# Kernel optimization log

Measured on AMD Instinct MI355X. Metric: run time of the kernel, lower is better.

Reference implementation:

```python
import jax, jax.numpy as jnp
import numpy as np

N_NODES = 100000


def gcn_conv(x, W, b, src, dst, norm, n_nodes):
    # x: [N, F_in] -> [N, F_out]; GCNConv: D^-1/2 (A+I) D^-1/2 (X W) + b
    h = x @ W                                   # [N, F_out]
    msg = h[src] * norm[:, None]                # [E+N, F_out] gather + scale
    out = jax.ops.segment_sum(msg, dst, num_segments=n_nodes)  # scatter-add
    return out + b


def setup_inputs() -> dict:
    key = jax.random.key(0)
    k0, k1, k2, k3, k4, k5 = jax.random.split(key, 6)
    n, e, f_in, f_hid, n_cls = N_NODES, 1600000, 128, 128, 3
    x = jax.random.normal(k0, (n, f_in), dtype=jnp.float32)
    edge_index = jax.random.randint(k1, (2, e), 0, n, dtype=jnp.int64)
    s1 = 1.0 / np.sqrt(f_in)
    s2 = 1.0 / np.sqrt(f_hid)
    W1 = jax.random.uniform(k2, (f_in, f_hid), jnp.float32, -s1, s1)
    b1 = jnp.zeros((f_hid,), jnp.float32)
    W2 = jax.random.uniform(k3, (f_hid, f_hid), jnp.float32, -s2, s2)
    b2 = jnp.zeros((f_hid,), jnp.float32)
    Wfc = jax.random.uniform(k4, (f_hid, n_cls), jnp.float32, -s2, s2)
    bfc = jax.random.uniform(k5, (n_cls,), jnp.float32, -s2, s2)
    return {"x": x, "edge_index": edge_index, "W1": W1, "b1": b1,
            "W2": W2, "b2": b2, "Wfc": Wfc, "bfc": bfc}


def reference(x, edge_index, W1, b1, W2, b2, Wfc, bfc):
    n = x.shape[0]
    # add self-loops (PyG GCNConv default add_self_loops=True)
    loops = jnp.arange(n, dtype=edge_index.dtype)
    src = jnp.concatenate([edge_index[0], loops])
    dst = jnp.concatenate([edge_index[1], loops])
    deg = jax.ops.segment_sum(jnp.ones_like(dst, dtype=x.dtype), dst,
                              num_segments=n)
    dinv = jax.lax.rsqrt(deg)                   # deg >= 1 due to self-loops
    norm = dinv[src] * dinv[dst]                # [E+N]
    h = jax.nn.relu(gcn_conv(x, W1, b1, src, dst, norm, n))   # dropout=eval id
    h = jax.nn.relu(gcn_conv(h, W2, b2, src, dst, norm, n))
    return jnp.tanh(h @ Wfc + bfc)              # [N, 3]
```

## Files before the change

### kernel.cpp

```cpp
#include <hip/hip_runtime.h>
#include <hip/hip_bf16.h>
#include <hip/hip_fp16.h>


#define NODE_F 128

typedef __attribute__((ext_vector_type(8))) short bf16x8;
typedef __attribute__((ext_vector_type(8))) unsigned short u16x8;
typedef __attribute__((ext_vector_type(4))) float f32x4;

__device__ inline unsigned short bf16_rn(float x) {
    unsigned u = __builtin_bit_cast(unsigned, x);
    unsigned r = (u + 0x7fffu + ((u >> 16) & 1u)) >> 16;
    return (unsigned short)r;
}
__device__ inline float bf16_to_f(unsigned short h) {
    unsigned u = (unsigned)h << 16;
    return __builtin_bit_cast(float, u);
}
__device__ inline void acc8_h(float a[8], uint4 v, float s) {
    unsigned vv[4] = {v.x, v.y, v.z, v.w};
    #pragma unroll
    for (int j = 0; j < 4; ++j) {
        float2 f = __half22float2(__builtin_bit_cast(__half2, vv[j]));
        a[2 * j]     += f.x * s;
        a[2 * j + 1] += f.y * s;
    }
}


__global__ __launch_bounds__(256) void wconv_kernel(const float* __restrict__ W1,
                                                    const float* __restrict__ W2,
                                                    unsigned short* __restrict__ WhiT,
                                                    unsigned short* __restrict__ WloT)
{
    const float* W = blockIdx.x ? W2 : W1;
    unsigned short* hiT = WhiT + blockIdx.x * 128 * 128;
    unsigned short* loT = WloT + blockIdx.x * 128 * 128;
    int tid = threadIdx.x;
    for (int i = tid; i < 128 * 128; i += 256) {
        int k = i >> 7, n = i & 127;
        float x = W[i];
        unsigned short hi = bf16_rn(x);
        float lo = x - bf16_to_f(hi);
        hiT[n * 128 + k] = hi;
        loT[n * 128 + k] = bf16_rn(lo);
    }
}


__global__ __launch_bounds__(256) void scan_block_kernel(
    const int* __restrict__ degE, int* __restrict__ rsA,
    int* __restrict__ bsum, int N)
{
    __shared__ int s[256];
    const int tid = threadIdx.x;
    const int idx = blockIdx.x * 1024 + tid * 4;
    int v0 = (idx + 0 < N) ? degE[idx + 0] : 0;
    int v1 = (idx + 1 < N) ? degE[idx + 1] : 0;
    int v2 = (idx + 2 < N) ? degE[idx + 2] : 0;
    int v3 = (idx + 3 < N) ? degE[idx + 3] : 0;
    int t = v0 + v1 + v2 + v3;
    s[tid] = t;
    __syncthreads();
    #pragma unroll
    for (int off = 1; off < 256; off <<= 1) {
        int x = (tid >= off) ? s[tid - off] : 0;
        __syncthreads();
        s[tid] += x;
        __syncthreads();
    }
    int excl = s[tid] - t;
    if (idx + 0 < N) rsA[idx + 0] = excl;
    if (idx + 1 < N) rsA[idx + 1] = excl + v0;
    if (idx + 2 < N) rsA[idx + 2] = excl + v0 + v1;
    if (idx + 3 < N) rsA[idx + 3] = excl + v0 + v1 + v2;
    if (tid == 255) bsum[blockIdx.x] = s[255];
}

__global__ __launch_bounds__(1024) void scan_tops_kernel(int* __restrict__ bsum, int nb) {
    __shared__ int s[1024];
    const int tid = threadIdx.x;
    int v = (tid < nb) ? bsum[tid] : 0;
    s[tid] = v;
    __syncthreads();
    #pragma unroll
    for (int off = 1; off < 1024; off <<= 1) {
        int x = (tid >= off) ? s[tid - off] : 0;
        __syncthreads();
        s[tid] += x;
        __syncthreads();
    }
    if (tid < nb) bsum[tid] = s[tid] - v;
}


__global__ __launch_bounds__(256) void finish_fill_kernel(
    const int* __restrict__ src, const int* __restrict__ dst,
    const unsigned short* __restrict__ rank,
    const int* __restrict__ rsA, const int* __restrict__ bsum,
    int* __restrict__ rsB, float* __restrict__ dinv,
    const int* __restrict__ degE, int* __restrict__ csr_src,
    int E, int N, int fill_blocks)
{
    if ((int)blockIdx.x < fill_blocks) {
        int e = blockIdx.x * 256 + threadIdx.x;
        if (e < E) {
            int d = dst[e];
            csr_src[rsA[d] + bsum[d >> 10] + (int)rank[e]] = src[e];
        }
    } else {
        int i = (blockIdx.x - fill_blocks) * 256 + threadIdx.x;
        if (i < N) {
            int rs = rsA[i] + bsum[i >> 10];
            rsB[i] = rs;
            dinv[i] = rsqrtf((float)degE[i] + 1.0f);
            if (i == N - 1) rsB[N] = rs + degE[i];
        }
    }
}


template<bool SCALE_OUT>
__device__ __forceinline__ void gemm_compute(
    const unsigned short* __restrict__ WhiT, const unsigned short* __restrict__ WloT,
    const float* __restrict__ dinv, __half* __restrict__ Hout, int N, int rbase,
    unsigned short* xhi, unsigned short* xlo)
{
    const int tid  = threadIdx.x;
    const int lane = tid & 63;
    const int w    = tid >> 6;

    bf16x8 bhi[2][4], blo[2][4];
    {
        int n0   = w * 32 + (lane & 15);
        int koct = (lane >> 4) * 8;
        #pragma unroll
        for (int nt = 0; nt < 2; ++nt) {
            #pragma unroll
            for (int kk = 0; kk < 4; ++kk) {
                size_t o = (size_t)(n0 + nt * 16) * 128 + kk * 32 + koct;
                bhi[nt][kk] = *reinterpret_cast<const bf16x8*>(WhiT + o);
                blo[nt][kk] = *reinterpret_cast<const bf16x8*>(WloT + o);
            }
        }
    }

    f32x4 acc[4][2];
    #pragma unroll
    for (int m = 0; m < 4; ++m)
        #pragma unroll
        for (int nt = 0; nt < 2; ++nt)
            acc[m][nt] = (f32x4){0.f, 0.f, 0.f, 0.f};

    #pragma unroll
    for (int kk = 0; kk < 4; ++kk) {
        #pragma unroll
        for (int m = 0; m < 4; ++m) {
            int row  = m * 16 + (lane & 15);
            int koff = kk * 64 + (lane >> 4) * 16;
            int byte = row * 256 + (koff ^ ((row & 7) << 4));
            bf16x8 ahi = *reinterpret_cast<const bf16x8*>(reinterpret_cast<char*>(xhi) + byte);
            bf16x8 alo = *reinterpret_cast<const bf16x8*>(reinterpret_cast<char*>(xlo) + byte);
            #pragma unroll
            for (int nt = 0; nt < 2; ++nt) {
                acc[m][nt] = __builtin_amdgcn_mfma_f32_16x16x32_bf16(ahi, bhi[nt][kk], acc[m][nt], 0, 0, 0);
                acc[m][nt] = __builtin_amdgcn_mfma_f32_16x16x32_bf16(ahi, blo[nt][kk], acc[m][nt], 0, 0, 0);
                acc[m][nt] = __builtin_amdgcn_mfma_f32_16x16x32_bf16(alo, bhi[nt][kk], acc[m][nt], 0, 0, 0);
            }
        }
    }

    #pragma unroll
    for (int m = 0; m < 4; ++m) {
        int row = rbase + m * 16 + (lane >> 4) * 4;
        int col = w * 32 + (lane & 15);
        #pragma unroll
        for (int nt = 0; nt < 2; ++nt) {
            #pragma unroll
            for (int r = 0; r < 4; ++r) {
                if (row + r < N) {
                    float v = acc[m][nt][r];
                    if (SCALE_OUT) v *= dinv[row + r];
                    Hout[(size_t)(row + r) * NODE_F + col + nt * 16] = __float2half(v);
                }
            }
        }
    }
}


__device__ __forceinline__ void gemm1_body(
    const float* __restrict__ Xf,
    const unsigned short* __restrict__ WhiT, const unsigned short* __restrict__ WloT,
    __half* __restrict__ Hout, int N, int bid,
    unsigned short* xhi, unsigned short* xlo)
{
    const int tid   = threadIdx.x;
    const int rbase = bid * 64;

    #pragma unroll
    for (int it = 0; it < 8; ++it) {
        int f   = it * 256 + tid;
        int row = f >> 5;
        int k4  = f & 31;
        float4 v = make_float4(0.f, 0.f, 0.f, 0.f);
        if (rbase + row < N)
            v = *reinterpret_cast<const float4*>(Xf + (size_t)(rbase + row) * NODE_F + k4 * 4);
        float xs[4] = {v.x, v.y, v.z, v.w};
        ushort4 h4, l4;
        unsigned short* hp = &h4.x;
        unsigned short* lp = &l4.x;
        #pragma unroll
        for (int j = 0; j < 4; ++j) {
            unsigned short hi = bf16_rn(xs[j]);
            hp[j] = hi;
            lp[j] = bf16_rn(xs[j] - bf16_to_f(hi));
        }
        int byte = row * 256 + ((k4 * 8) ^ ((row & 7) << 4));
        *reinterpret_cast<ushort4*>(reinterpret_cast<char*>(xhi) + byte) = h4;
        *reinterpret_cast<ushort4*>(reinterpret_cast<char*>(xlo) + byte) = l4;
    }
    __syncthreads();
    gemm_compute<false>(WhiT, WloT, nullptr, Hout, N, rbase, xhi, xlo);
}


__global__ __launch_bounds__(256) void gemm1deg_kernel(
    const int* __restrict__ dst, int* __restrict__ degE,
    unsigned short* __restrict__ rank, int E,
    int edge_blocks, int gemm_blocks,
    const float* __restrict__ X, const unsigned short* __restrict__ WhiT,
    const unsigned short* __restrict__ WloT, __half* __restrict__ H, int N)
{
    __shared__ unsigned short xhi[64 * 128];
    __shared__ unsigned short xlo[64 * 128];
    int q = blockIdx.x / 5, r = blockIdx.x % 5;
    if (r == 4) {
        int stride = edge_blocks * 256;
        for (int e = q * 256 + threadIdx.x; e < E; e += stride)
            rank[e] = (unsigned short)atomicAdd(&degE[dst[e]], 1);
    } else {
        int gid = q * 4 + r;
        if (gid < gemm_blocks)
            gemm1_body(X, WhiT, WloT, H, N, gid, xhi, xlo);
    }
}


template<bool EDGE_SCALE>
__device__ __forceinline__ void gather_core(
    const __half* __restrict__ Hs, const int* __restrict__ csr_src,
    const int* __restrict__ row_start, const float* __restrict__ dinv,
    int node, int ql, int qi, float a[8])
{
    const char* Hb = reinterpret_cast<const char*>(Hs);
    #pragma unroll
    for (int j = 0; j < 8; ++j) a[j] = 0.f;
    if (qi == 0) {
        float ds = EDGE_SCALE ? dinv[node] : 1.0f;
        acc8_h(a, *reinterpret_cast<const uint4*>(Hb + ((size_t)node * 256 + ql * 16)), ds);
    }

    int i   = row_start[node];
    int end = row_start[node + 1];
    for (; i + 7 < end; i += 8) {
        int s0 = csr_src[i + qi];
        int s1 = csr_src[i + 4 + qi];
        float d0 = EDGE_SCALE ? dinv[s0] : 1.0f;
        float d1 = EDGE_SCALE ? dinv[s1] : 1.0f;
        uint4 v0 = *reinterpret_cast<const uint4*>(Hb + ((size_t)s0 * 256 + ql * 16));
        uint4 v1 = *reinterpret_cast<const uint4*>(Hb + ((size_t)s1 * 256 + ql * 16));
        acc8_h(a, v0, d0);
        acc8_h(a, v1, d1);
    }
    for (; i < end; i += 4) {
        if (i + qi < end) {
            int s = csr_src[i + qi];
            float ds = EDGE_SCALE ? dinv[s] : 1.0f;
            acc8_h(a, *reinterpret_cast<const uint4*>(Hb + ((size_t)s * 256 + ql * 16)), ds);
        }
    }
    #pragma unroll
    for (int j = 0; j < 8; ++j) {
        a[j] += __shfl_xor(a[j], 32);
        a[j] += __shfl_xor(a[j], 16);
    }
}


__global__ __launch_bounds__(256) void gather1_kernel(
    const __half* __restrict__ H, const int* __restrict__ csr_src,
    const int* __restrict__ row_start, const float* __restrict__ dinv,
    const float* __restrict__ b, __half* __restrict__ A1, int N)
{
    int node = (blockIdx.x * blockDim.x + threadIdx.x) >> 6;
    int lane = threadIdx.x & 63;
    int ql = lane & 15, qi = lane >> 4;
    if (node >= N) return;

    float a[8];
    gather_core<true>(H, csr_src, row_start, dinv, node, ql, qi, a);

    if (qi == 0) {
        const float dd = dinv[node];
        u16x8 o;
        #pragma unroll
        for (int j = 0; j < 8; ++j) {
            float r = fmaxf(b[ql * 8 + j] + dd * a[j], 0.f);
            o[j] = __builtin_bit_cast(unsigned short, __float2half(r));
        }
        *reinterpret_cast<u16x8*>(reinterpret_cast<char*>(A1) + ((size_t)node * 256 + ql * 16)) = o;
    }
}


__global__ __launch_bounds__(256) void gemm2_kernel(
    const __half* __restrict__ A1,
    const unsigned short* __restrict__ WhiT, const unsigned short* __restrict__ WloT,
    const float* __restrict__ dinv, __half* __restrict__ Hs, int N)
{
    __shared__ unsigned short xhi[64 * 128];
    __shared__ unsigned short xlo[64 * 128];
    const int tid   = threadIdx.x;
    const int rbase = blockIdx.x * 64;

    #pragma unroll
    for (int it = 0; it < 4; ++it) {
        int idx = it * 256 + tid;
        int row = idx >> 4;
        int k8  = idx & 15;
        u16x8 h = {0, 0, 0, 0, 0, 0, 0, 0};
        u16x8 l = {0, 0, 0, 0, 0, 0, 0, 0};
        if (rbase + row < N) {
            u16x8 v = *reinterpret_cast<const u16x8*>(
                reinterpret_cast<const char*>(A1) + ((size_t)(rbase + row) * 256 + k8 * 16));
            #pragma unroll
            for (int j = 0; j < 8; ++j) {
                float f = __half2float(__builtin_bit_cast(__half, (unsigned short)v[j]));
                unsigned short hi = bf16_rn(f);
                h[j] = hi;
                l[j] = bf16_rn(f - bf16_to_f(hi));
            }
        }
        int byte = row * 256 + ((k8 * 16) ^ ((row & 7) << 4));
        *reinterpret_cast<u16x8*>(reinterpret_cast<char*>(xhi) + byte) = h;
        *reinterpret_cast<u16x8*>(reinterpret_cast<char*>(xlo) + byte) = l;
    }
    __syncthreads();
    gemm_compute<true>(WhiT, WloT, dinv, Hs, N, rbase, xhi, xlo);
}


__global__ __launch_bounds__(256) void gather2fc_kernel(
    const __half* __restrict__ Hs, const int* __restrict__ csr_src,
    const int* __restrict__ row_start, const float* __restrict__ dinv,
    const float* __restrict__ b, const float* __restrict__ Wfc,
    const float* __restrict__ bfc, float* __restrict__ out, int N)
{
    int node = (blockIdx.x * blockDim.x + threadIdx.x) >> 6;
    int lane = threadIdx.x & 63;
    int ql = lane & 15, qi = lane >> 4;
    if (node >= N) return;

    float a[8];
    gather_core<false>(Hs, csr_src, row_start, dinv, node, ql, qi, a);

    const float dd = dinv[node];
    float p0 = 0.f, p1 = 0.f, p2 = 0.f;
    #pragma unroll
    for (int j = 0; j < 8; ++j) {
        float r = fmaxf(b[ql * 8 + j] + dd * a[j], 0.f);
        const float* wr = Wfc + (size_t)(ql * 8 + j) * 3;
        p0 += r * wr[0]; p1 += r * wr[1]; p2 += r * wr[2];
    }
    #pragma unroll
    for (int off = 8; off > 0; off >>= 1) {
        p0 += __shfl_down(p0, off);
        p1 += __shfl_down(p1, off);
        p2 += __shfl_down(p2, off);
    }
    if (lane == 0) {
        out[(size_t)node * 3 + 0] = tanhf(p0 + bfc[0]);
        out[(size_t)node * 3 + 1] = tanhf(p1 + bfc[1]);
        out[(size_t)node * 3 + 2] = tanhf(p2 + bfc[2]);
    }
}

extern "C" void kernel_launch(void* const* d_in, const int* in_sizes, int n_in,
                              void* d_out, int out_size, void* d_ws, size_t ws_size,
                              hipStream_t stream)
{
    const float* x    = (const float*)d_in[0];
    const int*   edge = (const int*)d_in[1];
    const float* W1   = (const float*)d_in[2];
    const float* b1   = (const float*)d_in[3];
    const float* W2   = (const float*)d_in[4];
    const float* b2   = (const float*)d_in[5];
    const float* Wfc  = (const float*)d_in[6];
    const float* bfc  = (const float*)d_in[7];
    float* out = (float*)d_out;

    const int N = in_sizes[0] / NODE_F;
    const int E = in_sizes[1] / 2;
    const int* src = edge;
    const int* dst = edge + E;

    char* ws = (char*)d_ws;
    size_t off = 0;
    auto alloc = [&](size_t bytes) {
        void* p = ws + off;
        off += (bytes + 511) & ~511ull;
        return p;
    };
    const int nblk = (N + 1023) / 1024;
    float* dinv      = (float*)alloc((size_t)N * 4);
    int*   degE      = (int*)  alloc((size_t)N * 4);
    unsigned short* rank = (unsigned short*)alloc((size_t)E * 2);
    int*   rsA       = (int*)  alloc((size_t)N * 4);
    int*   rsB       = (int*)  alloc((size_t)(N + 1) * 4);
    int*   bsum      = (int*)  alloc((size_t)nblk * 4);
    int*   csr_src   = (int*)  alloc((size_t)E * 4);
    unsigned short* WhiT = (unsigned short*)alloc(2 * 128 * 128 * 2);
    unsigned short* WloT = (unsigned short*)alloc(2 * 128 * 128 * 2);
    __half* H        = (__half*)alloc((size_t)N * NODE_F * 2);
    __half* A1       = (__half*)alloc((size_t)N * NODE_F * 2);
    __half* H2       = (__half*)alloc((size_t)N * NODE_F * 2);
    (void)ws_size; (void)n_in; (void)out_size;

    const int B = 256;
    const int gemm_grid   = (N + 63) / 64;
    const int gather_grid = (N + 3) / 4;
    const int fill_blocks = (E + B - 1) / B;
    const int fin_blocks  = (N + B - 1) / B;

    const int edge_blocks  = (gemm_grid + 3) / 4;
    const int total_blocks = gemm_grid + edge_blocks + 4;

    wconv_kernel<<<2, B, 0, stream>>>(W1, W2, WhiT, WloT);
    hipMemsetAsync(degE, 0, (size_t)N * 4, stream);

    gemm1deg_kernel<<<total_blocks, B, 0, stream>>>(
        dst, degE, rank, E, edge_blocks, gemm_grid, x, WhiT, WloT, H, N);

    scan_block_kernel<<<nblk, B, 0, stream>>>(degE, rsA, bsum, N);
    scan_tops_kernel<<<1, 1024, 0, stream>>>(bsum, nblk);

    finish_fill_kernel<<<fill_blocks + fin_blocks, B, 0, stream>>>(
        src, dst, rank, rsA, bsum, rsB, dinv, degE, csr_src, E, N, fill_blocks);

    gather1_kernel<<<gather_grid, B, 0, stream>>>(H, csr_src, rsB, dinv, b1, A1, N);

    gemm2_kernel<<<gemm_grid, B, 0, stream>>>(A1, WhiT + 128 * 128, WloT + 128 * 128,
                                              dinv, H2, N);

    gather2fc_kernel<<<gather_grid, B, 0, stream>>>(H2, csr_src, rsB, dinv, b2,
                                                    Wfc, bfc, out, N);
}
```

Before: 301.7 us.

## Split degree atomics across eight planes and unroll gather loop by sixteen

Degree counting now spreads atomics over eight per-plane counter arrays, chosen by edge index, to reduce contention on the same address. The scan kernel turns the plane counts into per-plane prefix offsets, and the CSR fill adds the plane offset to compute each edge's slot. The cost is a memset eight times larger, extra scan reads and writes, and one more gather in the fill kernel. Separately, the gather loop gets a 16-edge unrolled body to keep more loads in flight.

```diff
diff --git a/kernel.cpp b/kernel.cpp
--- a/kernel.cpp
+++ b/kernel.cpp
@@ -4,6 +4,7 @@
 
 
 #define NODE_F 128
+#define NPLANE 8
 
 typedef __attribute__((ext_vector_type(8))) short bf16x8;
 typedef __attribute__((ext_vector_type(8))) unsigned short u16x8;
@@ -50,17 +51,31 @@
 
 
 __global__ __launch_bounds__(256) void scan_block_kernel(
-    const int* __restrict__ degE, int* __restrict__ rsA,
-    int* __restrict__ bsum, int N)
+    int* __restrict__ degP, int* __restrict__ degTot,
+    int* __restrict__ rsA, int* __restrict__ bsum, int N)
 {
     __shared__ int s[256];
     const int tid = threadIdx.x;
     const int idx = blockIdx.x * 1024 + tid * 4;
-    int v0 = (idx + 0 < N) ? degE[idx + 0] : 0;
-    int v1 = (idx + 1 < N) ? degE[idx + 1] : 0;
-    int v2 = (idx + 2 < N) ? degE[idx + 2] : 0;
-    int v3 = (idx + 3 < N) ? degE[idx + 3] : 0;
-    int t = v0 + v1 + v2 + v3;
+
+    int tot[4];
+    #pragma unroll
+    for (int j4 = 0; j4 < 4; ++j4) {
+        int node = idx + j4;
+        int t = 0;
+        if (node < N) {
+            #pragma unroll
+            for (int p = 0; p < NPLANE; ++p) {
+                int v = degP[(size_t)p * N + node];
+                degP[(size_t)p * N + node] = t;
+                t += v;
+            }
+            degTot[node] = t;
+        }
+        tot[j4] = (node < N) ? t : 0;
+    }
+
+    int t = tot[0] + tot[1] + tot[2] + tot[3];
     s[tid] = t;
     __syncthreads();
     #pragma unroll
@@ -72,9 +87,9 @@
     }
     int excl = s[tid] - t;
     if (idx + 0 < N) rsA[idx + 0] = excl;
-    if (idx + 1 < N) rsA[idx + 1] = excl + v0;
-    if (idx + 2 < N) rsA[idx + 2] = excl + v0 + v1;
-    if (idx + 3 < N) rsA[idx + 3] = excl + v0 + v1 + v2;
+    if (idx + 1 < N) rsA[idx + 1] = excl + tot[0];
+    if (idx + 2 < N) rsA[idx + 2] = excl + tot[0] + tot[1];
+    if (idx + 3 < N) rsA[idx + 3] = excl + tot[0] + tot[1] + tot[2];
     if (tid == 255) bsum[blockIdx.x] = s[255];
 }
 
@@ -99,23 +114,24 @@
     const int* __restrict__ src, const int* __restrict__ dst,
     const unsigned short* __restrict__ rank,
     const int* __restrict__ rsA, const int* __restrict__ bsum,
+    const int* __restrict__ degP, const int* __restrict__ degTot,
     int* __restrict__ rsB, float* __restrict__ dinv,
-    const int* __restrict__ degE, int* __restrict__ csr_src,
-    int E, int N, int fill_blocks)
+    int* __restrict__ csr_src, int E, int N, int fill_blocks)
 {
     if ((int)blockIdx.x < fill_blocks) {
         int e = blockIdx.x * 256 + threadIdx.x;
         if (e < E) {
             int d = dst[e];
-            csr_src[rsA[d] + bsum[d >> 10] + (int)rank[e]] = src[e];
+            int p = e & (NPLANE - 1);
+            csr_src[rsA[d] + bsum[d >> 10] + degP[(size_t)p * N + d] + (int)rank[e]] = src[e];
         }
     } else {
         int i = (blockIdx.x - fill_blocks) * 256 + threadIdx.x;
         if (i < N) {
             int rs = rsA[i] + bsum[i >> 10];
             rsB[i] = rs;
-            dinv[i] = rsqrtf((float)degE[i] + 1.0f);
-            if (i == N - 1) rsB[N] = rs + degE[i];
+            dinv[i] = rsqrtf((float)degTot[i] + 1.0f);
+            if (i == N - 1) rsB[N] = rs + degTot[i];
         }
     }
 }
@@ -227,7 +243,7 @@
 
 
 __global__ __launch_bounds__(256) void gemm1deg_kernel(
-    const int* __restrict__ dst, int* __restrict__ degE,
+    const int* __restrict__ dst, int* __restrict__ degP,
     unsigned short* __restrict__ rank, int E,
     int edge_blocks, int gemm_blocks,
     const float* __restrict__ X, const unsigned short* __restrict__ WhiT,
@@ -238,8 +254,10 @@
     int q = blockIdx.x / 5, r = blockIdx.x % 5;
     if (r == 4) {
         int stride = edge_blocks * 256;
-        for (int e = q * 256 + threadIdx.x; e < E; e += stride)
-            rank[e] = (unsigned short)atomicAdd(&degE[dst[e]], 1);
+        for (int e = q * 256 + threadIdx.x; e < E; e += stride) {
+            int p = e & (NPLANE - 1);
+            rank[e] = (unsigned short)atomicAdd(&degP[(size_t)p * N + dst[e]], 1);
+        }
     } else {
         int gid = q * 4 + r;
         if (gid < gemm_blocks)
@@ -264,6 +282,24 @@
 
     int i   = row_start[node];
     int end = row_start[node + 1];
+    for (; i + 15 < end; i += 16) {
+        int s0 = csr_src[i + qi];
+        int s1 = csr_src[i + 4 + qi];
+        int s2 = csr_src[i + 8 + qi];
+        int s3 = csr_src[i + 12 + qi];
+        float d0 = EDGE_SCALE ? dinv[s0] : 1.0f;
+        float d1 = EDGE_SCALE ? dinv[s1] : 1.0f;
+        float d2 = EDGE_SCALE ? dinv[s2] : 1.0f;
+        float d3 = EDGE_SCALE ? dinv[s3] : 1.0f;
+        uint4 v0 = *reinterpret_cast<const uint4*>(Hb + ((size_t)s0 * 256 + ql * 16));
+        uint4 v1 = *reinterpret_cast<const uint4*>(Hb + ((size_t)s1 * 256 + ql * 16));
+        uint4 v2 = *reinterpret_cast<const uint4*>(Hb + ((size_t)s2 * 256 + ql * 16));
+        uint4 v3 = *reinterpret_cast<const uint4*>(Hb + ((size_t)s3 * 256 + ql * 16));
+        acc8_h(a, v0, d0);
+        acc8_h(a, v1, d1);
+        acc8_h(a, v2, d2);
+        acc8_h(a, v3, d3);
+    }
     for (; i + 7 < end; i += 8) {
         int s0 = csr_src[i + qi];
         int s1 = csr_src[i + 4 + qi];
@@ -415,7 +451,8 @@
     };
     const int nblk = (N + 1023) / 1024;
     float* dinv      = (float*)alloc((size_t)N * 4);
-    int*   degE      = (int*)  alloc((size_t)N * 4);
+    int*   degP      = (int*)  alloc((size_t)NPLANE * N * 4);
+    int*   degTot    = (int*)  alloc((size_t)N * 4);
     unsigned short* rank = (unsigned short*)alloc((size_t)E * 2);
     int*   rsA       = (int*)  alloc((size_t)N * 4);
     int*   rsB       = (int*)  alloc((size_t)(N + 1) * 4);
@@ -438,16 +475,16 @@
     const int total_blocks = gemm_grid + edge_blocks + 4;
 
     wconv_kernel<<<2, B, 0, stream>>>(W1, W2, WhiT, WloT);
-    hipMemsetAsync(degE, 0, (size_t)N * 4, stream);
+    hipMemsetAsync(degP, 0, (size_t)NPLANE * N * 4, stream);
 
     gemm1deg_kernel<<<total_blocks, B, 0, stream>>>(
-        dst, degE, rank, E, edge_blocks, gemm_grid, x, WhiT, WloT, H, N);
-
-    scan_block_kernel<<<nblk, B, 0, stream>>>(degE, rsA, bsum, N);
+        dst, degP, rank, E, edge_blocks, gemm_grid, x, WhiT, WloT, H, N);
+
+    scan_block_kernel<<<nblk, B, 0, stream>>>(degP, degTot, rsA, bsum, N);
     scan_tops_kernel<<<1, 1024, 0, stream>>>(bsum, nblk);
 
     finish_fill_kernel<<<fill_blocks + fin_blocks, B, 0, stream>>>(
-        src, dst, rank, rsA, bsum, rsB, dinv, degE, csr_src, E, N, fill_blocks);
+        src, dst, rank, rsA, bsum, degP, degTot, rsB, dinv, csr_src, E, N, fill_blocks);
 
     gather1_kernel<<<gather_grid, B, 0, stream>>>(H, csr_src, rsB, dinv, b1, A1, N);
 
```

Result: slower. 311.9 us (+3.4%).

## Store features in 16-column slices so gathers hit a cache-resident slice

Applied to the files above, without the earlier changes.

Hidden features are written in a feature-sliced layout: eight contiguous slices of 16 half columns, each N×16. The gather kernels assign one slice per block, interleaved across blocks. Each block gathers 32-byte rows, so the working set per slice (about 3.2 MB) can stay in L2/LLC and random neighbor reads are meant to hit cache more often. The cost is many more, smaller 4-byte loads per lane, repeated index and dinv reads across the 8 slices, and an extra partial-output buffer plus a finalize kernel for the FC/tanh step.

```diff
diff --git a/kernel.cpp b/kernel.cpp
--- a/kernel.cpp
+++ b/kernel.cpp
@@ -17,15 +17,6 @@
 __device__ inline float bf16_to_f(unsigned short h) {
     unsigned u = (unsigned)h << 16;
     return __builtin_bit_cast(float, u);
-}
-__device__ inline void acc8_h(float a[8], uint4 v, float s) {
-    unsigned vv[4] = {v.x, v.y, v.z, v.w};
-    #pragma unroll
-    for (int j = 0; j < 4; ++j) {
-        float2 f = __half22float2(__builtin_bit_cast(__half2, vv[j]));
-        a[2 * j]     += f.x * s;
-        a[2 * j + 1] += f.y * s;
-    }
 }
 
 
@@ -177,12 +168,14 @@
         int col = w * 32 + (lane & 15);
         #pragma unroll
         for (int nt = 0; nt < 2; ++nt) {
+            int f = col + nt * 16;
+            __half* outp = Hout + (size_t)(f >> 4) * ((size_t)N * 16) + (f & 15);
             #pragma unroll
             for (int r = 0; r < 4; ++r) {
                 if (row + r < N) {
                     float v = acc[m][nt][r];
                     if (SCALE_OUT) v *= dinv[row + r];
-                    Hout[(size_t)(row + r) * NODE_F + col + nt * 16] = __float2half(v);
+                    outp[(size_t)(row + r) * 16] = __float2half(v);
                 }
             }
         }
@@ -249,68 +242,74 @@
 
 
 template<bool EDGE_SCALE>
-__device__ __forceinline__ void gather_core(
-    const __half* __restrict__ Hs, const int* __restrict__ csr_src,
+__device__ __forceinline__ void gather_slice(
+    const __half* __restrict__ Hsl, const int* __restrict__ csr_src,
     const int* __restrict__ row_start, const float* __restrict__ dinv,
-    int node, int ql, int qi, float a[8])
-{
-    const char* Hb = reinterpret_cast<const char*>(Hs);
-    #pragma unroll
-    for (int j = 0; j < 8; ++j) a[j] = 0.f;
-    if (qi == 0) {
+    int node, int g, int f2, float2& a)
+{
+    const unsigned* Hu = reinterpret_cast<const unsigned*>(Hsl);
+    a.x = 0.f; a.y = 0.f;
+    if (g == 0) {
         float ds = EDGE_SCALE ? dinv[node] : 1.0f;
-        acc8_h(a, *reinterpret_cast<const uint4*>(Hb + ((size_t)node * 256 + ql * 16)), ds);
-    }
-
+        float2 h = __half22float2(__builtin_bit_cast(__half2, Hu[(size_t)node * 8 + f2]));
+        a.x += h.x * ds; a.y += h.y * ds;
+    }
     int i   = row_start[node];
     int end = row_start[node + 1];
-    for (; i + 7 < end; i += 8) {
-        int s0 = csr_src[i + qi];
-        int s1 = csr_src[i + 4 + qi];
+    for (; i + 15 < end; i += 16) {
+        int s0 = csr_src[i + g];
+        int s1 = csr_src[i + 8 + g];
         float d0 = EDGE_SCALE ? dinv[s0] : 1.0f;
         float d1 = EDGE_SCALE ? dinv[s1] : 1.0f;
-        uint4 v0 = *reinterpret_cast<const uint4*>(Hb + ((size_t)s0 * 256 + ql * 16));
-        uint4 v1 = *reinterpret_cast<const uint4*>(Hb + ((size_t)s1 * 256 + ql * 16));
-        acc8_h(a, v0, d0);
-        acc8_h(a, v1, d1);
-    }
-    for (; i < end; i += 4) {
-        if (i + qi < end) {
-            int s = csr_src[i + qi];
+        unsigned v0 = Hu[(size_t)s0 * 8 + f2];
+        unsigned v1 = Hu[(size_t)s1 * 8 + f2];
+        float2 h0 = __half22float2(__builtin_bit_cast(__half2, v0));
+        float2 h1 = __half22float2(__builtin_bit_cast(__half2, v1));
+        a.x += h0.x * d0 + h1.x * d1;
+        a.y += h0.y * d0 + h1.y * d1;
+    }
+    for (; i < end; i += 8) {
+        if (i + g < end) {
+            int s = csr_src[i + g];
             float ds = EDGE_SCALE ? dinv[s] : 1.0f;
-            acc8_h(a, *reinterpret_cast<const uint4*>(Hb + ((size_t)s * 256 + ql * 16)), ds);
-        }
-    }
-    #pragma unroll
-    for (int j = 0; j < 8; ++j) {
-        a[j] += __shfl_xor(a[j], 32);
-        a[j] += __shfl_xor(a[j], 16);
-    }
-}
-
-
-__global__ __launch_bounds__(256) void gather1_kernel(
+            float2 h = __half22float2(__builtin_bit_cast(__half2, Hu[(size_t)s * 8 + f2]));
+            a.x += h.x * ds; a.y += h.y * ds;
+        }
+    }
+    a.x += __shfl_xor(a.x, 8);  a.y += __shfl_xor(a.y, 8);
+    a.x += __shfl_xor(a.x, 16); a.y += __shfl_xor(a.y, 16);
+    a.x += __shfl_xor(a.x, 32); a.y += __shfl_xor(a.y, 32);
+}
+
+#define NPW 4
+
+
+__global__ __launch_bounds__(256) void gather1s_kernel(
     const __half* __restrict__ H, const int* __restrict__ csr_src,
     const int* __restrict__ row_start, const float* __restrict__ dinv,
-    const float* __restrict__ b, __half* __restrict__ A1, int N)
-{
-    int node = (blockIdx.x * blockDim.x + threadIdx.x) >> 6;
-    int lane = threadIdx.x & 63;
-    int ql = lane & 15, qi = lane >> 4;
-    if (node >= N) return;
-
-    float a[8];
-    gather_core<true>(H, csr_src, row_start, dinv, node, ql, qi, a);
-
-    if (qi == 0) {
-        const float dd = dinv[node];
-        u16x8 o;
-        #pragma unroll
-        for (int j = 0; j < 8; ++j) {
-            float r = fmaxf(b[ql * 8 + j] + dd * a[j], 0.f);
-            o[j] = __builtin_bit_cast(unsigned short, __float2half(r));
-        }
-        *reinterpret_cast<u16x8*>(reinterpret_cast<char*>(A1) + ((size_t)node * 256 + ql * 16)) = o;
+    const float* __restrict__ b1, __half* __restrict__ A1, int N)
+{
+    const int slice = blockIdx.x & 7;
+    const int wave  = threadIdx.x >> 6;
+    const int lane  = threadIdx.x & 63;
+    const int g = lane >> 3, f2 = lane & 7;
+    const __half* Hsl = H  + (size_t)slice * ((size_t)N * 16);
+    unsigned*     Asl = reinterpret_cast<unsigned*>(A1) + (size_t)slice * ((size_t)N * 8);
+    const int base = ((blockIdx.x >> 3) * 4 + wave) * NPW;
+
+    for (int t = 0; t < NPW; ++t) {
+        int node = base + t;
+        if (node >= N) return;
+        float2 a;
+        gather_slice<true>(Hsl, csr_src, row_start, dinv, node, g, f2, a);
+        if (g == 0) {
+            float dd = dinv[node];
+            int f = slice * 16 + f2 * 2;
+            float r0 = fmaxf(b1[f]     + dd * a.x, 0.f);
+            float r1 = fmaxf(b1[f + 1] + dd * a.y, 0.f);
+            __half2 o = __float22half2_rn(make_float2(r0, r1));
+            Asl[(size_t)node * 8 + f2] = __builtin_bit_cast(unsigned, o);
+        }
     }
 }
 
@@ -333,8 +332,11 @@
         u16x8 h = {0, 0, 0, 0, 0, 0, 0, 0};
         u16x8 l = {0, 0, 0, 0, 0, 0, 0, 0};
         if (rbase + row < N) {
+            int slice = k8 >> 1;
+            int j0    = (k8 & 1) * 8;
             u16x8 v = *reinterpret_cast<const u16x8*>(
-                reinterpret_cast<const char*>(A1) + ((size_t)(rbase + row) * 256 + k8 * 16));
+                reinterpret_cast<const unsigned short*>(A1) +
+                (size_t)slice * ((size_t)N * 16) + (size_t)(rbase + row) * 16 + j0);
             #pragma unroll
             for (int j = 0; j < 8; ++j) {
                 float f = __half2float(__builtin_bit_cast(__half, (unsigned short)v[j]));
@@ -352,39 +354,59 @@
 }
 
 
-__global__ __launch_bounds__(256) void gather2fc_kernel(
+__global__ __launch_bounds__(256) void gather2fcs_kernel(
     const __half* __restrict__ Hs, const int* __restrict__ csr_src,
     const int* __restrict__ row_start, const float* __restrict__ dinv,
-    const float* __restrict__ b, const float* __restrict__ Wfc,
-    const float* __restrict__ bfc, float* __restrict__ out, int N)
-{
-    int node = (blockIdx.x * blockDim.x + threadIdx.x) >> 6;
-    int lane = threadIdx.x & 63;
-    int ql = lane & 15, qi = lane >> 4;
-    if (node >= N) return;
-
-    float a[8];
-    gather_core<false>(Hs, csr_src, row_start, dinv, node, ql, qi, a);
-
-    const float dd = dinv[node];
-    float p0 = 0.f, p1 = 0.f, p2 = 0.f;
-    #pragma unroll
-    for (int j = 0; j < 8; ++j) {
-        float r = fmaxf(b[ql * 8 + j] + dd * a[j], 0.f);
-        const float* wr = Wfc + (size_t)(ql * 8 + j) * 3;
-        p0 += r * wr[0]; p1 += r * wr[1]; p2 += r * wr[2];
-    }
-    #pragma unroll
-    for (int off = 8; off > 0; off >>= 1) {
-        p0 += __shfl_down(p0, off);
-        p1 += __shfl_down(p1, off);
-        p2 += __shfl_down(p2, off);
-    }
-    if (lane == 0) {
-        out[(size_t)node * 3 + 0] = tanhf(p0 + bfc[0]);
-        out[(size_t)node * 3 + 1] = tanhf(p1 + bfc[1]);
-        out[(size_t)node * 3 + 2] = tanhf(p2 + bfc[2]);
-    }
+    const float* __restrict__ b2, const float* __restrict__ Wfc,
+    float* __restrict__ outPart, int N)
+{
+    const int slice = blockIdx.x & 7;
+    const int wave  = threadIdx.x >> 6;
+    const int lane  = threadIdx.x & 63;
+    const int g = lane >> 3, f2 = lane & 7;
+    const __half* Hsl = Hs + (size_t)slice * ((size_t)N * 16);
+    const int base = ((blockIdx.x >> 3) * 4 + wave) * NPW;
+
+    for (int t = 0; t < NPW; ++t) {
+        int node = base + t;
+        if (node >= N) return;
+        float2 a;
+        gather_slice<false>(Hsl, csr_src, row_start, dinv, node, g, f2, a);
+        if (g == 0) {
+            float dd = dinv[node];
+            int f = slice * 16 + f2 * 2;
+            float r0 = fmaxf(b2[f]     + dd * a.x, 0.f);
+            float r1 = fmaxf(b2[f + 1] + dd * a.y, 0.f);
+            float p0 = r0 * Wfc[f * 3 + 0] + r1 * Wfc[(f + 1) * 3 + 0];
+            float p1 = r0 * Wfc[f * 3 + 1] + r1 * Wfc[(f + 1) * 3 + 1];
+            float p2 = r0 * Wfc[f * 3 + 2] + r1 * Wfc[(f + 1) * 3 + 2];
+            #pragma unroll
+            for (int off = 1; off < 8; off <<= 1) {
+                p0 += __shfl_xor(p0, off);
+                p1 += __shfl_xor(p1, off);
+                p2 += __shfl_xor(p2, off);
+            }
+            if (f2 == 0) {
+                float* op = outPart + ((size_t)slice * N + node) * 3;
+                op[0] = p0; op[1] = p1; op[2] = p2;
+            }
+        }
+    }
+}
+
+
+__global__ __launch_bounds__(256) void fc_finalize_kernel(
+    const float* __restrict__ outPart, const float* __restrict__ bfc,
+    float* __restrict__ out, int N)
+{
+    int i = blockIdx.x * 256 + threadIdx.x;
+    if (i >= N * 3) return;
+    int c = i % 3;
+    float s = bfc[c];
+    #pragma unroll
+    for (int sl = 0; sl < 8; ++sl)
+        s += outPart[(size_t)sl * ((size_t)N * 3) + i];
+    out[i] = tanhf(s);
 }
 
 extern "C" void kernel_launch(void* const* d_in, const int* in_sizes, int n_in,
@@ -426,13 +448,15 @@
     __half* H        = (__half*)alloc((size_t)N * NODE_F * 2);
     __half* A1       = (__half*)alloc((size_t)N * NODE_F * 2);
     __half* H2       = (__half*)alloc((size_t)N * NODE_F * 2);
+    float*  outPart  = (float*)alloc((size_t)8 * N * 3 * 4);
     (void)ws_size; (void)n_in; (void)out_size;
 
     const int B = 256;
     const int gemm_grid   = (N + 63) / 64;
-    const int gather_grid = (N + 3) / 4;
     const int fill_blocks = (E + B - 1) / B;
     const int fin_blocks  = (N + B - 1) / B;
+    const int node_chunks = (N + 4 * NPW - 1) / (4 * NPW);
+    const int gatherS_grid = node_chunks * 8;
 
     const int edge_blocks  = (gemm_grid + 3) / 4;
     const int total_blocks = gemm_grid + edge_blocks + 4;
@@ -449,11 +473,13 @@
     finish_fill_kernel<<<fill_blocks + fin_blocks, B, 0, stream>>>(
         src, dst, rank, rsA, bsum, rsB, dinv, degE, csr_src, E, N, fill_blocks);
 
-    gather1_kernel<<<gather_grid, B, 0, stream>>>(H, csr_src, rsB, dinv, b1, A1, N);
+    gather1s_kernel<<<gatherS_grid, B, 0, stream>>>(H, csr_src, rsB, dinv, b1, A1, N);
 
     gemm2_kernel<<<gemm_grid, B, 0, stream>>>(A1, WhiT + 128 * 128, WloT + 128 * 128,
                                               dinv, H2, N);
 
-    gather2fc_kernel<<<gather_grid, B, 0, stream>>>(H2, csr_src, rsB, dinv, b2,
-                                                    Wfc, bfc, out, N);
-}
+    gather2fcs_kernel<<<gatherS_grid, B, 0, stream>>>(H2, csr_src, rsB, dinv, b2,
+                                                      Wfc, outPart, N);
+
+    fc_finalize_kernel<<<(N * 3 + B - 1) / B, B, 0, stream>>>(outPart, bfc, out, N);
+}
```

After: 615.1 us. 2.04x slower.
